# Kernel optimization log

Measured on AMD Instinct MI355X. Metric: run time of the kernel, lower is better.

## Reference

```python
import jax, jax.numpy as jnp
import numpy as np

K_ORDER, NUM_HEADS, BETA = 4, 2, 0.5
D_IN, D_OUT = 64, 64


def _batch_and_pos(n_nodes, N):
    # batch[i] = graph id of node i; pos[i] = index of node i within its graph
    batch = jnp.repeat(jnp.arange(n_nodes.shape[0], dtype=jnp.int32), n_nodes, total_repeat_length=N)
    ptr = jnp.concatenate([jnp.zeros(1, jnp.int32), jnp.cumsum(n_nodes).astype(jnp.int32)])
    pos = jnp.arange(N, dtype=jnp.int32) - ptr[batch]
    return batch, pos


def _to_pad(feat, batch, pos, Bsz, max_node):
    out_shape = (Bsz, max_node) + feat.shape[1:]
    return jnp.zeros(out_shape, feat.dtype).at[batch, pos].set(feat)


def fast_attn_conv(qs, ks, vs, n_nodes, batch, pos, max_node):
    # qs/ks/vs: [N,H,D]; linear attention with per-graph kv outer-product sums
    Bsz = n_nodes.shape[0]
    q_pad = _to_pad(qs, batch, pos, Bsz, max_node)  # [B,M,H,D]
    k_pad = _to_pad(ks, batch, pos, Bsz, max_node)
    v_pad = _to_pad(vs, batch, pos, Bsz, max_node)
    kv = jnp.einsum('bnhd,bnhe->bdhe', k_pad, v_pad)  # [B,D,H,D]
    v_sum = jax.ops.segment_sum(vs, batch, num_segments=Bsz)  # [B,H,D]
    k_sum = jax.ops.segment_sum(ks, batch, num_segments=Bsz)  # [B,H,D]
    numerator = jnp.einsum('bnhd,bdhe->bnhe', q_pad, kv)[batch, pos] + v_sum[batch]
    denom = jnp.einsum('bnhd,bhd->bnh', q_pad, k_sum)[batch, pos]
    denom = denom + n_nodes.astype(qs.dtype)[batch][:, None]
    return numerator / denom[..., None]


def gcn_conv(x, edge_index, e_feat):
    # x: [N,H,D], e_feat: [E,D]
    N = x.shape[0]
    row, col = edge_index[0], edge_index[1]
    deg = jax.ops.segment_sum(jnp.ones(row.shape[0], x.dtype), row, num_segments=N)
    dis = jnp.where(deg > 0, deg ** -0.5, jnp.zeros_like(deg))
    w = dis[row] * dis[col]  # [E]
    msg_edge = jax.ops.segment_sum(w[:, None] * e_feat, row, num_segments=N)  # [N,D]
    new_feat = jax.ops.segment_sum(x[col] * w[:, None, None], row, num_segments=N)  # [N,H,D]
    return new_feat + msg_edge[:, None, :]


def setup_inputs():
    key = jax.random.key(0)
    ks = jax.random.split(key, 10)
    B = 64
    n_nodes_np = np.tile(np.array([1000, 2000], np.int32), B // 2)  # sums to 96000
    N = int(n_nodes_np.sum())
    E = 768000
    x = jax.random.normal(ks[0], (N, D_IN), jnp.float32)
    edge_index = jax.random.randint(ks[1], (2, E), 0, N, jnp.int32)
    edge_attr = jax.random.randint(ks[2], (E, 3), 0, 8, jnp.int32)
    s = 0.02
    Wq_w = jax.random.normal(ks[3], (D_IN * NUM_HEADS, D_IN), jnp.float32) * s
    Wq_b = jnp.zeros((D_IN * NUM_HEADS,), jnp.float32)
    Wk_w = jax.random.normal(ks[4], (D_IN * NUM_HEADS, D_IN), jnp.float32) * s
    Wk_b = jnp.zeros((D_IN * NUM_HEADS,), jnp.float32)
    Wo_w = jax.random.normal(ks[5], (D_OUT, D_IN * NUM_HEADS), jnp.float32) * s
    Wo_b = jnp.zeros((D_OUT,), jnp.float32)
    bond_emb = jax.random.normal(ks[6], (3, 8, D_OUT), jnp.float32) * s
    return {"x": x, "Wq_w": Wq_w, "Wq_b": Wq_b, "Wk_w": Wk_w, "Wk_b": Wk_b,
            "Wo_w": Wo_w, "Wo_b": Wo_b, "bond_emb": bond_emb,
            "edge_index": edge_index, "edge_attr": edge_attr,
            "n_nodes": jnp.asarray(n_nodes_np)}


def reference(x, Wq_w, Wq_b, Wk_w, Wk_b, Wo_w, Wo_b, bond_emb, edge_index, edge_attr, n_nodes):
    N = x.shape[0]
    max_node = 2000  # static max over n_nodes
    batch, pos = _batch_and_pos(n_nodes, N)
    query = (x @ Wq_w.T + Wq_b).reshape(N, NUM_HEADS, D_IN)
    key_t = (x @ Wk_w.T + Wk_b).reshape(N, NUM_HEADS, D_IN)
    qs = query / jnp.linalg.norm(query, axis=2, keepdims=True)
    kk = key_t / jnp.linalg.norm(key_t, axis=2, keepdims=True)
    # BondEncoder: sum of per-feature embeddings
    e_feat = bond_emb[0][edge_attr[:, 0]] + bond_emb[1][edge_attr[:, 1]] + bond_emb[2][edge_attr[:, 2]]
    h = jnp.broadcast_to(x[:, None, :], (N, NUM_HEADS, D_IN))
    acc = h
    cur = h
    for _ in range(K_ORDER):
        gcn_i = gcn_conv(cur, edge_index, e_feat)
        attn_i = fast_attn_conv(qs, kk, cur, n_nodes, batch, pos, max_node)
        cur = BETA * gcn_i + (1.0 - BETA) * attn_i
        acc = acc + cur
    out = acc.reshape(N, NUM_HEADS * D_IN)
    return (out @ Wo_w.T + Wo_b) / NUM_HEADS
```

## Files before the change

### kernel.cpp

```cpp
#include <hip/hip_runtime.h>
#include <hip/hip_bf16.h>


typedef __attribute__((ext_vector_type(8))) short bf16x8;
typedef __attribute__((ext_vector_type(4))) float f32x4v;

#define CHUNK 128

__device__ __forceinline__ float asf(unsigned int u) { union { unsigned int i; float f; } v; v.i = u; return v.f; }
__device__ __forceinline__ float b2f_u(unsigned short u) { return asf((unsigned int)u << 16); }
__device__ __forceinline__ unsigned short f2b_u(float f) {
    __hip_bfloat16 h = __float2bfloat16(f);
    union { __hip_bfloat16 h; unsigned short u; } v; v.h = h; return v.u;
}
__device__ __forceinline__ unsigned int pack2(float a, float b) {
    return (unsigned int)f2b_u(a) | ((unsigned int)f2b_u(b) << 16);
}
__device__ __forceinline__ unsigned int add5(unsigned int a, unsigned int b,
                                             unsigned int c, unsigned int d, unsigned int e) {
    float lo = asf(a << 16) + asf(b << 16) + asf(c << 16) + asf(d << 16) + asf(e << 16);
    float hi = asf(a & 0xffff0000u) + asf(b & 0xffff0000u) + asf(c & 0xffff0000u)
             + asf(d & 0xffff0000u) + asf(e & 0xffff0000u);
    return pack2(lo, hi);
}
__device__ __forceinline__ float wave_reduce_sum(float v) {
    #pragma unroll
    for (int off = 32; off > 0; off >>= 1) v += __shfl_xor(v, off, 64);
    return v;
}

__global__ void k_ptr(const int* __restrict__ nn, int* __restrict__ ptr,
                      int* __restrict__ cptr, int* __restrict__ tptr, int B) {
    if (threadIdx.x == 0 && blockIdx.x == 0) {
        int s = 0, c = 0, t = 0; ptr[0] = 0; cptr[0] = 0; tptr[0] = 0;
        for (int i = 0; i < B; ++i) {
            s += nn[i]; ptr[i + 1] = s;
            c += (nn[i] + CHUNK - 1) / CHUNK; cptr[i + 1] = c;
            t += (nn[i] + 15) / 16; tptr[i + 1] = t;
        }
    }
}

__global__ void k_batch(const int* __restrict__ ptr, int* __restrict__ batch) {
    int b = blockIdx.x;
    int s = ptr[b], e = ptr[b + 1];
    for (int i = s + threadIdx.x; i < e; i += blockDim.x) batch[i] = b;
}

__global__ void k_wcvt(const float* __restrict__ Wq_w, const float* __restrict__ Wk_w,
                       const float* __restrict__ Wo_w, unsigned short* __restrict__ Wb) {
    int i = blockIdx.x * 256 + threadIdx.x;
    if (i < 24576) {
        float v = (i < 8192) ? Wq_w[i] : ((i < 16384) ? Wk_w[i - 8192] : Wo_w[i - 16384]);
        Wb[i] = f2b_u(v);
    }
}

__global__ __launch_bounds__(256) void k_qkm(
    const float* __restrict__ x, const unsigned short* __restrict__ Wb,
    const float* __restrict__ Wq_b, const float* __restrict__ Wk_b,
    unsigned short* __restrict__ q, unsigned short* __restrict__ kq,
    unsigned short* __restrict__ x0, int N)
{
    __shared__ unsigned short sbuf[4][16][72];
    int w = threadIdx.x >> 6, l = threadIdx.x & 63;
    int six = l & 15, quad = l >> 4;
    int base = (blockIdx.x * 4 + w) * 16;
    if (base >= N) return;
    int n = base + six;
    int nc = min(n, N - 1);
    int r0 = l >> 3, m = l & 7;

    const float* xr = x + (size_t)nc * 64;
    float4 xa = *(const float4*)(xr + quad * 8);
    float4 xb = *(const float4*)(xr + quad * 8 + 4);
    float4 xc = *(const float4*)(xr + 32 + quad * 8);
    float4 xd = *(const float4*)(xr + 32 + quad * 8 + 4);
    union { bf16x8 v; unsigned int u[4]; } b0, b1;
    b0.u[0] = pack2(xa.x, xa.y); b0.u[1] = pack2(xa.z, xa.w);
    b0.u[2] = pack2(xb.x, xb.y); b0.u[3] = pack2(xb.z, xb.w);
    b1.u[0] = pack2(xc.x, xc.y); b1.u[1] = pack2(xc.z, xc.w);
    b1.u[2] = pack2(xd.x, xd.y); b1.u[3] = pack2(xd.z, xd.w);

    *(uint4*)&sbuf[w][six][quad * 8]      = make_uint4(b0.u[0], b0.u[1], b0.u[2], b0.u[3]);
    *(uint4*)&sbuf[w][six][32 + quad * 8] = make_uint4(b1.u[0], b1.u[1], b1.u[2], b1.u[3]);
    __builtin_amdgcn_wave_barrier();
    #pragma unroll
    for (int c = 0; c < 2; ++c) {
        int r = r0 + c * 8;
        int n2 = base + r;
        if (n2 < N)
            *(uint4*)(x0 + (size_t)n2 * 64 + m * 8) = *(const uint4*)&sbuf[w][r][m * 8];
    }
    __builtin_amdgcn_wave_barrier();

    #pragma unroll
    for (int g = 0; g < 4; ++g) {
        f32x4v c[4];
        #pragma unroll
        for (int tt = 0; tt < 4; ++tt) {
            int t = g * 4 + tt;
            const unsigned short* wr = Wb + (size_t)(t * 16 + six) * 64;
            bf16x8 a0 = *(const bf16x8*)(wr + quad * 8);
            bf16x8 a1 = *(const bf16x8*)(wr + 32 + quad * 8);
            f32x4v cc = {0.f, 0.f, 0.f, 0.f};
            cc = __builtin_amdgcn_mfma_f32_16x16x32_bf16(a0, b0.v, cc, 0, 0, 0);
            cc = __builtin_amdgcn_mfma_f32_16x16x32_bf16(a1, b1.v, cc, 0, 0, 0);
            c[tt] = cc;
        }
        const float* bias = (g < 2) ? Wq_b : Wk_b;
        int cb = (g & 1) * 64 + quad * 4;
        float ss = 0.f;
        #pragma unroll
        for (int tt = 0; tt < 4; ++tt) {
            float4 bv = *(const float4*)(bias + cb + tt * 16);
            c[tt][0] += bv.x; c[tt][1] += bv.y; c[tt][2] += bv.z; c[tt][3] += bv.w;
            ss += c[tt][0] * c[tt][0] + c[tt][1] * c[tt][1]
                + c[tt][2] * c[tt][2] + c[tt][3] * c[tt][3];
        }
        ss += __shfl_xor(ss, 16, 64);
        ss += __shfl_xor(ss, 32, 64);
        float sc = rsqrtf(ss);
        #pragma unroll
        for (int tt = 0; tt < 4; ++tt) {
            unsigned int u0 = pack2(c[tt][0] * sc, c[tt][1] * sc);
            unsigned int u1 = pack2(c[tt][2] * sc, c[tt][3] * sc);
            *(uint2*)&sbuf[w][six][tt * 16 + quad * 4] = make_uint2(u0, u1);
        }
        __builtin_amdgcn_wave_barrier();
        unsigned short* arr = (g < 2) ? q : kq;
        #pragma unroll
        for (int c2 = 0; c2 < 2; ++c2) {
            int r = r0 + c2 * 8;
            int n2 = base + r;
            if (n2 < N)
                *(uint4*)(arr + (size_t)n2 * 128 + (g & 1) * 64 + m * 8)
                    = *(const uint4*)&sbuf[w][r][m * 8];
        }
        __builtin_amdgcn_wave_barrier();
    }
}

__global__ void k_deg(const int* __restrict__ row, int* __restrict__ deg,
                      int* __restrict__ slot, int E) {
    int e = blockIdx.x * 256 + threadIdx.x;
    if (e < E) slot[e] = atomicAdd(&deg[row[e]], 1);
}

__global__ void k_scan1(const int* __restrict__ deg, int* __restrict__ rowstart,
                        int* __restrict__ bsum, float* __restrict__ dis, int N) {
    __shared__ int sh[256];
    int t = threadIdx.x, n = blockIdx.x * 256 + t;
    int v = (n < N) ? deg[n] : 0;
    if (n < N) dis[n] = v > 0 ? rsqrtf((float)v) : 0.f;
    sh[t] = v; __syncthreads();
    #pragma unroll
    for (int off = 1; off < 256; off <<= 1) {
        int add = (t >= off) ? sh[t - off] : 0;
        __syncthreads();
        sh[t] += add;
        __syncthreads();
    }
    if (n < N) rowstart[n] = sh[t] - v;
    if (t == 255) bsum[blockIdx.x] = sh[255];
}

__global__ void k_scan2(int* __restrict__ bsum, int nb) {
    __shared__ int sh[512];
    __shared__ int carry;
    int t = threadIdx.x;
    if (t == 0) carry = 0;
    __syncthreads();
    for (int base = 0; base < nb; base += 512) {
        int idx = base + t;
        int v = (idx < nb) ? bsum[idx] : 0;
        sh[t] = v; __syncthreads();
        for (int off = 1; off < 512; off <<= 1) {
            int add = (t >= off) ? sh[t - off] : 0;
            __syncthreads();
            sh[t] += add;
            __syncthreads();
        }
        if (idx < nb) bsum[idx] = sh[t] - v + carry;
        __syncthreads();
        if (t == 0) carry += sh[511];
        __syncthreads();
    }
}

__global__ void k_scan3(int* __restrict__ rowstart, const int* __restrict__ bsum, int N, int E) {
    int n = blockIdx.x * 256 + threadIdx.x;
    if (n < N) rowstart[n] += bsum[blockIdx.x];
    if (n == 0) rowstart[N] = E;
}

__global__ void k_fill(const int* __restrict__ eidx, const float* __restrict__ dis,
                       const int* __restrict__ rowstart, const int* __restrict__ slot,
                       int4* __restrict__ csr_pack, const int* __restrict__ eattr, int E) {
    int e = blockIdx.x * 256 + threadIdx.x;
    if (e >= E) return;
    int r = eidx[e], c = eidx[E + e];
    float wv = dis[r] * dis[c];
    int a0 = eattr[e * 3 + 0], a1 = eattr[e * 3 + 1], a2 = eattr[e * 3 + 2];
    int idx = rowstart[r] + slot[e];
    int4 v;
    v.x = c;
    v.y = __float_as_int(wv);
    v.z = a0 | (a1 << 8) | (a2 << 16);
    v.w = 0;
    csr_pack[idx] = v;
}

__global__ __launch_bounds__(256) void k_msg(
    const int* __restrict__ rowstart, const int4* __restrict__ csr_pack,
    const float* __restrict__ bond, unsigned short* __restrict__ msgb, int N) {
    __shared__ float bl[1536];
    int t = threadIdx.x, w = t >> 6, l = t & 63;
    for (int i = t; i < 1536; i += 256) bl[i] = bond[i];
    __syncthreads();
    for (int n = blockIdx.x * 4 + w; n < N; n += gridDim.x * 4) {
        int s0 = rowstart[n], s1 = rowstart[n + 1];
        float m = 0.f;
        #pragma unroll 4
        for (int i = s0; i < s1; ++i) {
            int4 pk = csr_pack[i];
            float wv = __int_as_float(pk.y);
            int att = pk.z;
            m += wv * (bl[(att & 255) * 64 + l] + bl[(8 + ((att >> 8) & 255)) * 64 + l]
                     + bl[(16 + (att >> 16)) * 64 + l]);
        }
        msgb[(size_t)n * 64 + l] = f2b_u(m);
    }
}

__global__ __launch_bounds__(256) void k_ksump(
    const unsigned short* __restrict__ kq, const int* __restrict__ ptr,
    const int* __restrict__ cptr, float* __restrict__ partKS, int B)
{
    int cid = blockIdx.x;
    if (cid >= cptr[B]) return;
    int lo = 0, hi = B - 1;
    while (lo < hi) { int mid = (lo + hi + 1) >> 1; if (cptr[mid] <= cid) lo = mid; else hi = mid - 1; }
    int b = lo;
    int start = ptr[b] + (cid - cptr[b]) * CHUNK;
    int end = min(start + CHUNK, ptr[b + 1]);
    int t = threadIdx.x, r = t >> 7, col = t & 127;
    float a = 0.f;
    for (int n = start + r; n < end; n += 2)
        a += b2f_u(kq[(size_t)n * 128 + col]);
    __shared__ float sh[256];
    sh[t] = a;
    __syncthreads();
    if (t < 128) partKS[(size_t)cid * 128 + t] = sh[t] + sh[t + 128];
}

__global__ __launch_bounds__(128) void k_ksr(
    const float* __restrict__ partKS, const int* __restrict__ cptr,
    float* __restrict__ ksum, int B)
{
    int b = blockIdx.x, t = threadIdx.x;
    float s = 0.f;
    int c0 = cptr[b], c1 = cptr[b + 1];
    for (int c = c0; c < c1; ++c) s += partKS[(size_t)c * 128 + t];
    ksum[b * 128 + t] = s;
}

__global__ __launch_bounds__(256) void k_denom(
    const unsigned short* __restrict__ q, const float* __restrict__ ksum,
    const int* __restrict__ batch, const int* __restrict__ nn,
    float* __restrict__ denom, int N)
{
    int w = threadIdx.x >> 6, l = threadIdx.x & 63;
    int n = blockIdx.x * 4 + w;
    if (n >= N) return;
    int b = batch[n];
    float d0 = b2f_u(q[(size_t)n * 128 + l]) * ksum[b * 128 + l];
    float d1 = b2f_u(q[(size_t)n * 128 + 64 + l]) * ksum[b * 128 + 64 + l];
    d0 = wave_reduce_sum(d0);
    d1 = wave_reduce_sum(d1);
    if (l == 0) {
        float nf = (float)nn[b];
        denom[n * 2 + 0] = d0 + nf;
        denom[n * 2 + 1] = d1 + nf;
    }
}

__global__ __launch_bounds__(256) void k_kvp(
    const unsigned short* __restrict__ kq, const unsigned short* __restrict__ cur,
    int pitch, int hoff,
    const int* __restrict__ ptr, const int* __restrict__ cptr,
    unsigned short* __restrict__ partKV, float* __restrict__ partVS, int B)
{
    int cid = blockIdx.x;
    if (cid >= cptr[B]) return;
    int lo = 0, hi = B - 1;
    while (lo < hi) { int mid = (lo + hi + 1) >> 1; if (cptr[mid] <= cid) lo = mid; else hi = mid - 1; }
    int b = lo;
    int start = ptr[b] + (cid - cptr[b]) * CHUNK;
    int end = min(start + CHUNK, ptr[b + 1]);

    int w = threadIdx.x >> 6, l = threadIdx.x & 63;
    int h = w >> 1, dhalf = w & 1;
    int six = l & 15, quad = l >> 4;

    f32x4v c00 = {0,0,0,0}, c01 = {0,0,0,0}, c10 = {0,0,0,0}, c11 = {0,0,0,0};
    f32x4v c20 = {0,0,0,0}, c21 = {0,0,0,0}, c30 = {0,0,0,0}, c31 = {0,0,0,0};
    f32x4v s0 = {0,0,0,0}, s1 = {0,0,0,0}, s2 = {0,0,0,0}, s3 = {0,0,0,0};

    const unsigned short ONE = 0x3F80;

    for (int nb = start; nb < end; nb += 32) {
        union { bf16x8 v; unsigned short s[8]; } a0u, a1u, a2u, a3u, b0u, b1u, onu;
        if (nb + 32 <= end) {
            const unsigned short* vb = cur + (size_t)(nb + quad * 8) * pitch + h * hoff + six;
            const unsigned short* kb = kq  + (size_t)(nb + quad * 8) * 128 + h * 64 + dhalf * 32 + six;
            #pragma unroll
            for (int j = 0; j < 8; ++j) {
                a0u.s[j] = vb[j * pitch];
                a1u.s[j] = vb[j * pitch + 16];
                a2u.s[j] = vb[j * pitch + 32];
                a3u.s[j] = vb[j * pitch + 48];
                b0u.s[j] = kb[j * 128];
                b1u.s[j] = kb[j * 128 + 16];
                onu.s[j] = ONE;
            }
        } else {
            #pragma unroll
            for (int j = 0; j < 8; ++j) {
                int nd = nb + quad * 8 + j;
                int ndc = min(nd, end - 1);
                bool ok = nd < end;
                const unsigned short* vb = cur + (size_t)ndc * pitch + h * hoff + six;
                const unsigned short* kb = kq  + (size_t)ndc * 128 + h * 64 + dhalf * 32 + six;
                a0u.s[j] = vb[0];
                a1u.s[j] = vb[16];
                a2u.s[j] = vb[32];
                a3u.s[j] = vb[48];
                b0u.s[j] = ok ? kb[0]  : (unsigned short)0;
                b1u.s[j] = ok ? kb[16] : (unsigned short)0;
                onu.s[j] = ok ? ONE : (unsigned short)0;
            }
        }
        c00 = __builtin_amdgcn_mfma_f32_16x16x32_bf16(a0u.v, b0u.v, c00, 0, 0, 0);
        c01 = __builtin_amdgcn_mfma_f32_16x16x32_bf16(a0u.v, b1u.v, c01, 0, 0, 0);
        c10 = __builtin_amdgcn_mfma_f32_16x16x32_bf16(a1u.v, b0u.v, c10, 0, 0, 0);
        c11 = __builtin_amdgcn_mfma_f32_16x16x32_bf16(a1u.v, b1u.v, c11, 0, 0, 0);
        c20 = __builtin_amdgcn_mfma_f32_16x16x32_bf16(a2u.v, b0u.v, c20, 0, 0, 0);
        c21 = __builtin_amdgcn_mfma_f32_16x16x32_bf16(a2u.v, b1u.v, c21, 0, 0, 0);
        c30 = __builtin_amdgcn_mfma_f32_16x16x32_bf16(a3u.v, b0u.v, c30, 0, 0, 0);
        c31 = __builtin_amdgcn_mfma_f32_16x16x32_bf16(a3u.v, b1u.v, c31, 0, 0, 0);
        s0  = __builtin_amdgcn_mfma_f32_16x16x32_bf16(a0u.v, onu.v, s0, 0, 0, 0);
        s1  = __builtin_amdgcn_mfma_f32_16x16x32_bf16(a1u.v, onu.v, s1, 0, 0, 0);
        s2  = __builtin_amdgcn_mfma_f32_16x16x32_bf16(a2u.v, onu.v, s2, 0, 0, 0);
        s3  = __builtin_amdgcn_mfma_f32_16x16x32_bf16(a3u.v, onu.v, s3, 0, 0, 0);
    }

    unsigned short* dst = partKV + (size_t)cid * 8192 + h * 4096 + dhalf * 32 + six;
    #pragma unroll
    for (int r = 0; r < 4; ++r) {
        int e = quad * 4 + r;
        dst[(e +  0) * 64 +  0] = f2b_u(c00[r]);
        dst[(e +  0) * 64 + 16] = f2b_u(c01[r]);
        dst[(e + 16) * 64 +  0] = f2b_u(c10[r]);
        dst[(e + 16) * 64 + 16] = f2b_u(c11[r]);
        dst[(e + 32) * 64 +  0] = f2b_u(c20[r]);
        dst[(e + 32) * 64 + 16] = f2b_u(c21[r]);
        dst[(e + 48) * 64 +  0] = f2b_u(c30[r]);
        dst[(e + 48) * 64 + 16] = f2b_u(c31[r]);
    }
    if (dhalf == 0 && six == 0) {
        float* vdst = partVS + (size_t)cid * 128 + h * 64;
        #pragma unroll
        for (int r = 0; r < 4; ++r) {
            int e = quad * 4 + r;
            vdst[e]      = s0[r];
            vdst[e + 16] = s1[r];
            vdst[e + 32] = s2[r];
            vdst[e + 48] = s3[r];
        }
    }
}

__global__ __launch_bounds__(256) void k_red(
    const unsigned short* __restrict__ partKV, const float* __restrict__ partVS,
    const int* __restrict__ cptr, unsigned short* __restrict__ kvT_b,
    float* __restrict__ vsum, int B)
{
    int bid = blockIdx.x;
    int gh = bid >> 1, half = bid & 1;
    int g = gh >> 1, h = gh & 1;
    int c0 = cptr[g], c1 = cptr[g + 1];
    int t = threadIdx.x;
    int off = half * 2048 + t * 8;
    float s[8];
    #pragma unroll
    for (int i = 0; i < 8; ++i) s[i] = 0.f;
    for (int c = c0; c < c1; ++c) {
        uint4 u = *(const uint4*)(partKV + (size_t)c * 8192 + h * 4096 + off);
        s[0] += asf(u.x << 16); s[1] += asf(u.x & 0xffff0000u);
        s[2] += asf(u.y << 16); s[3] += asf(u.y & 0xffff0000u);
        s[4] += asf(u.z << 16); s[5] += asf(u.z & 0xffff0000u);
        s[6] += asf(u.w << 16); s[7] += asf(u.w & 0xffff0000u);
    }
    unsigned int u[4];
    #pragma unroll
    for (int i = 0; i < 4; ++i) u[i] = pack2(s[2 * i], s[2 * i + 1]);
    *(uint4*)(kvT_b + (size_t)gh * 4096 + off) = make_uint4(u[0], u[1], u[2], u[3]);
    if (half == 0 && t < 64) {
        float vs = 0.f;
        for (int c = c0; c < c1; ++c) vs += partVS[(size_t)c * 128 + h * 64 + t];
        vsum[g * 128 + h * 64 + t] = vs;
    }
}

__global__ __launch_bounds__(256) void k_attn(
    const unsigned short* __restrict__ q, const unsigned short* __restrict__ kvT,
    const float* __restrict__ vsum, const float* __restrict__ denom,
    const int* __restrict__ ptr, const int* __restrict__ tptr,
    const unsigned short* __restrict__ msgb,
    unsigned short* __restrict__ curB, int B)
{
    int w = threadIdx.x >> 6, l = threadIdx.x & 63;
    int tid = blockIdx.x * 4 + w;
    if (tid >= tptr[B]) return;
    int lo = 0, hi = B - 1;
    while (lo < hi) { int mid = (lo + hi + 1) >> 1; if (tptr[mid] <= tid) lo = mid; else hi = mid - 1; }
    int b0 = lo;
    int start = ptr[b0] + (tid - tptr[b0]) * 16;
    int end = min(start + 16, ptr[b0 + 1]);
    int quad = l >> 4, six = l & 15;
    int n = start + six;
    int nc = min(n, end - 1);
    bool live = n < end;
    const unsigned short* mrow = msgb + (size_t)nc * 64;
    uint2 me[4];
    #pragma unroll
    for (int et = 0; et < 4; ++et) me[et] = *(const uint2*)(mrow + et * 16 + quad * 4);
    #pragma unroll
    for (int h = 0; h < 2; ++h) {
        const unsigned short* qrow = q + (size_t)nc * 128 + h * 64;
        bf16x8 qb0 = *(const bf16x8*)(qrow + quad * 8);
        bf16x8 qb1 = *(const bf16x8*)(qrow + 32 + quad * 8);
        const unsigned short* Bb = kvT + (size_t)(b0 * 2 + h) * 4096;
        float dn = denom[nc * 2 + h];
        const float* vsb = vsum + (b0 * 2 + h) * 64;
        #pragma unroll
        for (int et = 0; et < 4; ++et) {
            const unsigned short* arow = Bb + (size_t)(et * 16 + six) * 64;
            bf16x8 a0 = *(const bf16x8*)(arow + quad * 8);
            bf16x8 a1 = *(const bf16x8*)(arow + 32 + quad * 8);
            f32x4v c = {0.f, 0.f, 0.f, 0.f};
            c = __builtin_amdgcn_mfma_f32_16x16x32_bf16(a0, qb0, c, 0, 0, 0);
            c = __builtin_amdgcn_mfma_f32_16x16x32_bf16(a1, qb1, c, 0, 0, 0);
            float4 vs = *(const float4*)(vsb + et * 16 + quad * 4);
            float m0 = asf(me[et].x << 16), m1 = asf(me[et].x & 0xffff0000u);
            float m2 = asf(me[et].y << 16), m3 = asf(me[et].y & 0xffff0000u);
            float v0 = 0.5f * (c[0] + vs.x) / dn + 0.5f * m0;
            float v1 = 0.5f * (c[1] + vs.y) / dn + 0.5f * m1;
            float v2 = 0.5f * (c[2] + vs.z) / dn + 0.5f * m2;
            float v3 = 0.5f * (c[3] + vs.w) / dn + 0.5f * m3;
            if (live) {
                uint2 st = make_uint2(pack2(v0, v1), pack2(v2, v3));
                *(uint2*)(curB + (size_t)n * 128 + h * 64 + et * 16 + quad * 4) = st;
            }
        }
    }
}

__global__ __launch_bounds__(256) void k_gcn(
    const unsigned short* __restrict__ src, int pitch,
    const int* __restrict__ rowstart, const int4* __restrict__ csr_pack,
    unsigned short* __restrict__ curB, int N)
{
    int orig = blockIdx.x, nwg = gridDim.x;
    int q8 = nwg >> 3, r8 = nwg & 7;
    int xcd = orig & 7, jj = orig >> 3;
    int swz = (xcd < r8 ? xcd * (q8 + 1) : r8 * (q8 + 1) + (xcd - r8) * q8) + jj;

    int w = threadIdx.x >> 6, l = threadIdx.x & 63;
    int qq = l >> 4, ql = l & 15;
    int half = qq >> 1;
    int par  = qq & 1;
    int nA = swz * 8 + w * 2;
    if (nA >= N) return;
    bool hasB = (nA + 1) < N;
    int myN = nA + half;
    bool live = myN < N;
    int s0  = rowstart[nA];
    int sA1 = rowstart[nA + 1];
    int s1  = hasB ? rowstart[nA + 2] : sA1;
    int base = half ? sA1 : s0;
    int lim  = half ? s1  : sA1;

    int e0 = 8 * ql + par * 4;
    size_t o = (size_t)myN * 128 + e0;
    uint2 ub = make_uint2(0, 0);
    if (live) ub = *(const uint2*)(curB + o);

    int colofs = (8 * ql) & (pitch - 1);
    float g[8];
    #pragma unroll
    for (int j = 0; j < 8; ++j) g[j] = 0.f;
    const int2* cw2 = (const int2*)csr_pack;
    #pragma unroll 2
    for (int i = base + par; i < lim; i += 2) {
        int2 cw = cw2[2 * i];
        float wv = __int_as_float(cw.y);
        uint4 u = *(const uint4*)(src + (size_t)cw.x * pitch + colofs);
        g[0] += wv * asf(u.x << 16); g[1] += wv * asf(u.x & 0xffff0000u);
        g[2] += wv * asf(u.y << 16); g[3] += wv * asf(u.y & 0xffff0000u);
        g[4] += wv * asf(u.z << 16); g[5] += wv * asf(u.z & 0xffff0000u);
        g[6] += wv * asf(u.w << 16); g[7] += wv * asf(u.w & 0xffff0000u);
    }
    #pragma unroll
    for (int j = 0; j < 8; ++j) g[j] += __shfl_xor(g[j], 16, 64);
    float s0v = par ? g[4] : g[0];
    float s1v = par ? g[5] : g[1];
    float s2v = par ? g[6] : g[2];
    float s3v = par ? g[7] : g[3];
    if (live) {
        float v0 = 0.5f * s0v + asf(ub.x << 16);
        float v1 = 0.5f * s1v + asf(ub.x & 0xffff0000u);
        float v2 = 0.5f * s2v + asf(ub.y << 16);
        float v3 = 0.5f * s3v + asf(ub.y & 0xffff0000u);
        *(uint2*)(curB + o) = make_uint2(pack2(v0, v1), pack2(v2, v3));
    }
}

__global__ __launch_bounds__(256) void k_outm(
    const unsigned short* __restrict__ c0, const unsigned short* __restrict__ c1,
    const unsigned short* __restrict__ c2, const unsigned short* __restrict__ c3,
    const unsigned short* __restrict__ x0, const unsigned short* __restrict__ Wob,
    const float* __restrict__ Wo_b, float* __restrict__ out, int N)
{
    int w = threadIdx.x >> 6, l = threadIdx.x & 63;
    int six = l & 15, quad = l >> 4;
    int base = (blockIdx.x * 4 + w) * 16;
    if (base >= N) return;
    int n = base + six;
    int nc = min(n, N - 1);
    const unsigned short* xr = x0 + (size_t)nc * 64;
    uint4 xlo = *(const uint4*)(xr + quad * 8);
    uint4 xhi = *(const uint4*)(xr + 32 + quad * 8);
    union { bf16x8 v; unsigned int u[4]; } bfrag[4];
    #pragma unroll
    for (int f = 0; f < 4; ++f) {
        size_t off = (size_t)nc * 128 + f * 32 + quad * 8;
        uint4 u0 = *(const uint4*)(c0 + off);
        uint4 u1 = *(const uint4*)(c1 + off);
        uint4 u2 = *(const uint4*)(c2 + off);
        uint4 u3 = *(const uint4*)(c3 + off);
        uint4 xa = (f & 1) ? xhi : xlo;
        bfrag[f].u[0] = add5(xa.x, u0.x, u1.x, u2.x, u3.x);
        bfrag[f].u[1] = add5(xa.y, u0.y, u1.y, u2.y, u3.y);
        bfrag[f].u[2] = add5(xa.z, u0.z, u1.z, u2.z, u3.z);
        bfrag[f].u[3] = add5(xa.w, u0.w, u1.w, u2.w, u3.w);
    }
    #pragma unroll
    for (int t = 0; t < 4; ++t) {
        const unsigned short* wr = Wob + (size_t)(t * 16 + six) * 128;
        bf16x8 a0 = *(const bf16x8*)(wr + quad * 8);
        bf16x8 a1 = *(const bf16x8*)(wr + 32 + quad * 8);
        bf16x8 a2 = *(const bf16x8*)(wr + 64 + quad * 8);
        bf16x8 a3 = *(const bf16x8*)(wr + 96 + quad * 8);
        f32x4v c = {0.f, 0.f, 0.f, 0.f};
        c = __builtin_amdgcn_mfma_f32_16x16x32_bf16(a0, bfrag[0].v, c, 0, 0, 0);
        c = __builtin_amdgcn_mfma_f32_16x16x32_bf16(a1, bfrag[1].v, c, 0, 0, 0);
        c = __builtin_amdgcn_mfma_f32_16x16x32_bf16(a2, bfrag[2].v, c, 0, 0, 0);
        c = __builtin_amdgcn_mfma_f32_16x16x32_bf16(a3, bfrag[3].v, c, 0, 0, 0);
        if (n < N) {
            float4 bias = *(const float4*)(Wo_b + t * 16 + quad * 4);
            float4 o4;
            o4.x = (c[0] + bias.x) * 0.5f;
            o4.y = (c[1] + bias.y) * 0.5f;
            o4.z = (c[2] + bias.z) * 0.5f;
            o4.w = (c[3] + bias.w) * 0.5f;
            *(float4*)(out + (size_t)n * 64 + t * 16 + quad * 4) = o4;
        }
    }
}

extern "C" void kernel_launch(void* const* d_in, const int* in_sizes, int n_in,
                              void* d_out, int out_size, void* d_ws, size_t ws_size,
                              hipStream_t stream) {
    const float* x    = (const float*)d_in[0];
    const float* Wq_w = (const float*)d_in[1];
    const float* Wq_b = (const float*)d_in[2];
    const float* Wk_w = (const float*)d_in[3];
    const float* Wk_b = (const float*)d_in[4];
    const float* Wo_w = (const float*)d_in[5];
    const float* Wo_b = (const float*)d_in[6];
    const float* bond = (const float*)d_in[7];
    const int*   eidx = (const int*)d_in[8];
    const int*   eattr= (const int*)d_in[9];
    const int*   nn   = (const int*)d_in[10];
    float* out = (float*)d_out;
    int N = in_sizes[0] / 64;
    int E = in_sizes[9] / 3;
    int B = in_sizes[10];

    char* p = (char*)d_ws;
    auto alloc = [&](size_t bytes) { char* r = p; p += (bytes + 255) & ~(size_t)255; return r; };
    unsigned short* q    = (unsigned short*)alloc((size_t)N * 128 * 2);
    unsigned short* kq   = (unsigned short*)alloc((size_t)N * 128 * 2);
    unsigned short* x0   = (unsigned short*)alloc((size_t)N * 64 * 2);
    unsigned short* cur[4];
    for (int i = 0; i < 4; ++i) cur[i] = (unsigned short*)alloc((size_t)N * 128 * 2);
    int maxchunks = (N + CHUNK - 1) / CHUNK + B;
    int maxtiles  = (N + 15) / 16 + B;
    unsigned short* partKV = (unsigned short*)alloc((size_t)maxchunks * 8192 * 2);
    float* partVS = (float*)alloc((size_t)maxchunks * 128 * 4);
    float* partKS = (float*)alloc((size_t)maxchunks * 128 * 4);
    unsigned short* kvT_b = (unsigned short*)alloc((size_t)B * 2 * 64 * 64 * 2);
    float* vsum  = (float*)alloc((size_t)B * 128 * 4);
    float* ksum  = (float*)alloc((size_t)B * 128 * 4);
    float* denom = (float*)alloc((size_t)N * 2 * 4);
    float* dis   = (float*)alloc((size_t)N * 4);
    int* deg     = (int*)alloc((size_t)N * 4);
    int* rowstart= (int*)alloc((size_t)(N + 1) * 4);
    int* slot    = (int*)alloc((size_t)E * 4);
    int4* csr_pack = (int4*)alloc((size_t)E * 16);
    int* batch   = (int*)alloc((size_t)N * 4);
    int* ptr     = (int*)alloc((size_t)(B + 1) * 4);
    int* cptr    = (int*)alloc((size_t)(B + 1) * 4);
    int* tptr    = (int*)alloc((size_t)(B + 1) * 4);
    unsigned short* Wb = (unsigned short*)alloc(24576 * 2);
    int nb = (N + 255) / 256;
    int* bsum    = (int*)alloc((size_t)nb * 4);
    unsigned short* msgb = (unsigned short*)out;

    hipMemsetAsync(deg, 0, (size_t)N * 4, stream);

    k_ptr  <<<1, 64, 0, stream>>>(nn, ptr, cptr, tptr, B);
    k_batch<<<B, 256, 0, stream>>>(ptr, batch);
    k_wcvt <<<96, 256, 0, stream>>>(Wq_w, Wk_w, Wo_w, Wb);
    k_qkm  <<<(N + 63) / 64, 256, 0, stream>>>(x, Wb, Wq_b, Wk_b, q, kq, x0, N);
    k_deg  <<<(E + 255) / 256, 256, 0, stream>>>(eidx, deg, slot, E);
    k_scan1<<<nb, 256, 0, stream>>>(deg, rowstart, bsum, dis, N);
    k_scan2<<<1, 512, 0, stream>>>(bsum, nb);
    k_scan3<<<nb, 256, 0, stream>>>(rowstart, bsum, N, E);
    k_fill <<<(E + 255) / 256, 256, 0, stream>>>(eidx, dis, rowstart, slot, csr_pack, eattr, E);
    k_msg  <<<2048, 256, 0, stream>>>(rowstart, csr_pack, bond, msgb, N);
    k_ksump<<<maxchunks, 256, 0, stream>>>(kq, ptr, cptr, partKS, B);
    k_ksr  <<<B, 128, 0, stream>>>(partKS, cptr, ksum, B);
    k_denom<<<(N + 3) / 4, 256, 0, stream>>>(q, ksum, batch, nn, denom, N);

    int gcnblk = (N + 7) / 8;
    for (int it = 0; it < 4; ++it) {
        const unsigned short* src = (it == 0) ? x0 : cur[it - 1];
        int pitch = (it == 0) ? 64 : 128;
        int hoff  = (it == 0) ? 0 : 64;
        k_kvp <<<maxchunks, 256, 0, stream>>>(kq, src, pitch, hoff, ptr, cptr, partKV, partVS, B);
        k_red <<<B * 4, 256, 0, stream>>>(partKV, partVS, cptr, kvT_b, vsum, B);
        k_attn<<<(maxtiles + 3) / 4, 256, 0, stream>>>(q, kvT_b, vsum, denom, ptr, tptr, msgb, cur[it], B);
        k_gcn <<<gcnblk, 256, 0, stream>>>(src, pitch, rowstart, csr_pack, cur[it], N);
    }
    k_outm<<<(N + 63) / 64, 256, 0, stream>>>(cur[0], cur[1], cur[2], cur[3], x0, Wb + 16384, Wo_b, out, N);
}
```

Measured before the change: 657.5 us.

## Fuse denominator into attention kernel and compact GCN edge list to int2

Removes the separate k_denom and k_batch kernels. Each attention tile now computes the q·ksum denominator itself with a 16-element dot product and two cross-lane shuffles. k_msg also writes a compact 8-byte (col, weight) array, which k_gcn reads instead of the strided 16-byte CSR entries, cutting gather traffic in the four GCN passes. The cost is recomputing the denominator in every iteration (four times instead of once) and an extra E*8 byte write during message construction.

```diff
diff --git a/kernel.cpp b/kernel.cpp
--- a/kernel.cpp
+++ b/kernel.cpp
@@ -22,11 +22,6 @@
     float hi = asf(a & 0xffff0000u) + asf(b & 0xffff0000u) + asf(c & 0xffff0000u)
              + asf(d & 0xffff0000u) + asf(e & 0xffff0000u);
     return pack2(lo, hi);
-}
-__device__ __forceinline__ float wave_reduce_sum(float v) {
-    #pragma unroll
-    for (int off = 32; off > 0; off >>= 1) v += __shfl_xor(v, off, 64);
-    return v;
 }
 
 __global__ void k_ptr(const int* __restrict__ nn, int* __restrict__ ptr,
@@ -39,12 +34,6 @@
             t += (nn[i] + 15) / 16; tptr[i + 1] = t;
         }
     }
-}
-
-__global__ void k_batch(const int* __restrict__ ptr, int* __restrict__ batch) {
-    int b = blockIdx.x;
-    int s = ptr[b], e = ptr[b + 1];
-    for (int i = s + threadIdx.x; i < e; i += blockDim.x) batch[i] = b;
 }
 
 __global__ void k_wcvt(const float* __restrict__ Wq_w, const float* __restrict__ Wk_w,
@@ -213,7 +202,8 @@
 
 __global__ __launch_bounds__(256) void k_msg(
     const int* __restrict__ rowstart, const int4* __restrict__ csr_pack,
-    const float* __restrict__ bond, unsigned short* __restrict__ msgb, int N) {
+    const float* __restrict__ bond, unsigned short* __restrict__ msgb,
+    int2* __restrict__ cw8, int N) {
     __shared__ float bl[1536];
     int t = threadIdx.x, w = t >> 6, l = t & 63;
     for (int i = t; i < 1536; i += 256) bl[i] = bond[i];
@@ -226,6 +216,7 @@
             int4 pk = csr_pack[i];
             float wv = __int_as_float(pk.y);
             int att = pk.z;
+            if (l == 0) cw8[i] = make_int2(pk.x, pk.y);
             m += wv * (bl[(att & 255) * 64 + l] + bl[(8 + ((att >> 8) & 255)) * 64 + l]
                      + bl[(16 + (att >> 16)) * 64 + l]);
         }
@@ -263,26 +254,6 @@
     int c0 = cptr[b], c1 = cptr[b + 1];
     for (int c = c0; c < c1; ++c) s += partKS[(size_t)c * 128 + t];
     ksum[b * 128 + t] = s;
-}
-
-__global__ __launch_bounds__(256) void k_denom(
-    const unsigned short* __restrict__ q, const float* __restrict__ ksum,
-    const int* __restrict__ batch, const int* __restrict__ nn,
-    float* __restrict__ denom, int N)
-{
-    int w = threadIdx.x >> 6, l = threadIdx.x & 63;
-    int n = blockIdx.x * 4 + w;
-    if (n >= N) return;
-    int b = batch[n];
-    float d0 = b2f_u(q[(size_t)n * 128 + l]) * ksum[b * 128 + l];
-    float d1 = b2f_u(q[(size_t)n * 128 + 64 + l]) * ksum[b * 128 + 64 + l];
-    d0 = wave_reduce_sum(d0);
-    d1 = wave_reduce_sum(d1);
-    if (l == 0) {
-        float nf = (float)nn[b];
-        denom[n * 2 + 0] = d0 + nf;
-        denom[n * 2 + 1] = d1 + nf;
-    }
 }
 
 __global__ __launch_bounds__(256) void k_kvp(
@@ -415,7 +386,8 @@
 
 __global__ __launch_bounds__(256) void k_attn(
     const unsigned short* __restrict__ q, const unsigned short* __restrict__ kvT,
-    const float* __restrict__ vsum, const float* __restrict__ denom,
+    const float* __restrict__ vsum, const float* __restrict__ ksum,
+    const int* __restrict__ nn,
     const int* __restrict__ ptr, const int* __restrict__ tptr,
     const unsigned short* __restrict__ msgb,
     unsigned short* __restrict__ curB, int B)
@@ -432,6 +404,7 @@
     int n = start + six;
     int nc = min(n, end - 1);
     bool live = n < end;
+    float nf = (float)nn[b0];
     const unsigned short* mrow = msgb + (size_t)nc * 64;
     uint2 me[4];
     #pragma unroll
@@ -439,10 +412,26 @@
     #pragma unroll
     for (int h = 0; h < 2; ++h) {
         const unsigned short* qrow = q + (size_t)nc * 128 + h * 64;
-        bf16x8 qb0 = *(const bf16x8*)(qrow + quad * 8);
-        bf16x8 qb1 = *(const bf16x8*)(qrow + 32 + quad * 8);
+        union { bf16x8 v; unsigned short s[8]; } qb0, qb1;
+        qb0.v = *(const bf16x8*)(qrow + quad * 8);
+        qb1.v = *(const bf16x8*)(qrow + 32 + quad * 8);
+        const float* ksb = ksum + b0 * 128 + h * 64;
+        float4 ka = *(const float4*)(ksb + quad * 8);
+        float4 kb = *(const float4*)(ksb + quad * 8 + 4);
+        float4 kc = *(const float4*)(ksb + 32 + quad * 8);
+        float4 kd = *(const float4*)(ksb + 32 + quad * 8 + 4);
+        float dp = b2f_u(qb0.s[0]) * ka.x + b2f_u(qb0.s[1]) * ka.y
+                 + b2f_u(qb0.s[2]) * ka.z + b2f_u(qb0.s[3]) * ka.w
+                 + b2f_u(qb0.s[4]) * kb.x + b2f_u(qb0.s[5]) * kb.y
+                 + b2f_u(qb0.s[6]) * kb.z + b2f_u(qb0.s[7]) * kb.w
+                 + b2f_u(qb1.s[0]) * kc.x + b2f_u(qb1.s[1]) * kc.y
+                 + b2f_u(qb1.s[2]) * kc.z + b2f_u(qb1.s[3]) * kc.w
+                 + b2f_u(qb1.s[4]) * kd.x + b2f_u(qb1.s[5]) * kd.y
+                 + b2f_u(qb1.s[6]) * kd.z + b2f_u(qb1.s[7]) * kd.w;
+        dp += __shfl_xor(dp, 16, 64);
+        dp += __shfl_xor(dp, 32, 64);
+        float dn = dp + nf;
         const unsigned short* Bb = kvT + (size_t)(b0 * 2 + h) * 4096;
-        float dn = denom[nc * 2 + h];
         const float* vsb = vsum + (b0 * 2 + h) * 64;
         #pragma unroll
         for (int et = 0; et < 4; ++et) {
@@ -450,8 +439,8 @@
             bf16x8 a0 = *(const bf16x8*)(arow + quad * 8);
             bf16x8 a1 = *(const bf16x8*)(arow + 32 + quad * 8);
             f32x4v c = {0.f, 0.f, 0.f, 0.f};
-            c = __builtin_amdgcn_mfma_f32_16x16x32_bf16(a0, qb0, c, 0, 0, 0);
-            c = __builtin_amdgcn_mfma_f32_16x16x32_bf16(a1, qb1, c, 0, 0, 0);
+            c = __builtin_amdgcn_mfma_f32_16x16x32_bf16(a0, qb0.v, c, 0, 0, 0);
+            c = __builtin_amdgcn_mfma_f32_16x16x32_bf16(a1, qb1.v, c, 0, 0, 0);
             float4 vs = *(const float4*)(vsb + et * 16 + quad * 4);
             float m0 = asf(me[et].x << 16), m1 = asf(me[et].x & 0xffff0000u);
             float m2 = asf(me[et].y << 16), m3 = asf(me[et].y & 0xffff0000u);
@@ -469,7 +458,7 @@
 
 __global__ __launch_bounds__(256) void k_gcn(
     const unsigned short* __restrict__ src, int pitch,
-    const int* __restrict__ rowstart, const int4* __restrict__ csr_pack,
+    const int* __restrict__ rowstart, const int2* __restrict__ cw8,
     unsigned short* __restrict__ curB, int N)
 {
     int orig = blockIdx.x, nwg = gridDim.x;
@@ -501,10 +490,9 @@
     float g[8];
     #pragma unroll
     for (int j = 0; j < 8; ++j) g[j] = 0.f;
-    const int2* cw2 = (const int2*)csr_pack;
     #pragma unroll 2
     for (int i = base + par; i < lim; i += 2) {
-        int2 cw = cw2[2 * i];
+        int2 cw = cw8[i];
         float wv = __int_as_float(cw.y);
         uint4 u = *(const uint4*)(src + (size_t)cw.x * pitch + colofs);
         g[0] += wv * asf(u.x << 16); g[1] += wv * asf(u.x & 0xffff0000u);
@@ -614,13 +602,12 @@
     unsigned short* kvT_b = (unsigned short*)alloc((size_t)B * 2 * 64 * 64 * 2);
     float* vsum  = (float*)alloc((size_t)B * 128 * 4);
     float* ksum  = (float*)alloc((size_t)B * 128 * 4);
-    float* denom = (float*)alloc((size_t)N * 2 * 4);
     float* dis   = (float*)alloc((size_t)N * 4);
     int* deg     = (int*)alloc((size_t)N * 4);
     int* rowstart= (int*)alloc((size_t)(N + 1) * 4);
     int* slot    = (int*)alloc((size_t)E * 4);
     int4* csr_pack = (int4*)alloc((size_t)E * 16);
-    int* batch   = (int*)alloc((size_t)N * 4);
+    int2* cw8    = (int2*)alloc((size_t)E * 8);
     int* ptr     = (int*)alloc((size_t)(B + 1) * 4);
     int* cptr    = (int*)alloc((size_t)(B + 1) * 4);
     int* tptr    = (int*)alloc((size_t)(B + 1) * 4);
@@ -632,7 +619,6 @@
     hipMemsetAsync(deg, 0, (size_t)N * 4, stream);
 
     k_ptr  <<<1, 64, 0, stream>>>(nn, ptr, cptr, tptr, B);
-    k_batch<<<B, 256, 0, stream>>>(ptr, batch);
     k_wcvt <<<96, 256, 0, stream>>>(Wq_w, Wk_w, Wo_w, Wb);
     k_qkm  <<<(N + 63) / 64, 256, 0, stream>>>(x, Wb, Wq_b, Wk_b, q, kq, x0, N);
     k_deg  <<<(E + 255) / 256, 256, 0, stream>>>(eidx, deg, slot, E);
@@ -640,10 +626,9 @@
     k_scan2<<<1, 512, 0, stream>>>(bsum, nb);
     k_scan3<<<nb, 256, 0, stream>>>(rowstart, bsum, N, E);
     k_fill <<<(E + 255) / 256, 256, 0, stream>>>(eidx, dis, rowstart, slot, csr_pack, eattr, E);
-    k_msg  <<<2048, 256, 0, stream>>>(rowstart, csr_pack, bond, msgb, N);
+    k_msg  <<<2048, 256, 0, stream>>>(rowstart, csr_pack, bond, msgb, cw8, N);
     k_ksump<<<maxchunks, 256, 0, stream>>>(kq, ptr, cptr, partKS, B);
     k_ksr  <<<B, 128, 0, stream>>>(partKS, cptr, ksum, B);
-    k_denom<<<(N + 3) / 4, 256, 0, stream>>>(q, ksum, batch, nn, denom, N);
 
     int gcnblk = (N + 7) / 8;
     for (int it = 0; it < 4; ++it) {
@@ -652,8 +637,8 @@
         int hoff  = (it == 0) ? 0 : 64;
         k_kvp <<<maxchunks, 256, 0, stream>>>(kq, src, pitch, hoff, ptr, cptr, partKV, partVS, B);
         k_red <<<B * 4, 256, 0, stream>>>(partKV, partVS, cptr, kvT_b, vsum, B);
-        k_attn<<<(maxtiles + 3) / 4, 256, 0, stream>>>(q, kvT_b, vsum, denom, ptr, tptr, msgb, cur[it], B);
-        k_gcn <<<gcnblk, 256, 0, stream>>>(src, pitch, rowstart, csr_pack, cur[it], N);
+        k_attn<<<(maxtiles + 3) / 4, 256, 0, stream>>>(q, kvT_b, vsum, ksum, nn, ptr, tptr, msgb, cur[it], B);
+        k_gcn <<<gcnblk, 256, 0, stream>>>(src, pitch, rowstart, cw8, cur[it], N);
     }
     k_outm<<<(N + 63) / 64, 256, 0, stream>>>(cur[0], cur[1], cur[2], cur[3], x0, Wb + 16384, Wo_b, out, N);
 }
```

Measured after the change: 696.9 us. 6.0% more time.
